# Kernel tuning notes

Hardware: AMD Instinct MI355X
Metric: run time of the kernel (lower is better)

Reference implementation:

```python
import jax, jax.numpy as jnp
import numpy as np

NUM_GROUPS = 8
NUM_HEADS = 8
EPS = 1e-5


def setup_inputs() -> dict:
    key = jax.random.key(0)
    k1, k2, k3 = jax.random.split(key, 3)
    b, c, h, w = 16, 512, 32, 32
    x = jax.random.normal(k1, (b, c, h, w), dtype=jnp.float32)
    gn_w = jnp.ones((c,), dtype=jnp.float32)
    gn_b = jnp.zeros((c,), dtype=jnp.float32)
    qkv_w = jax.random.normal(k2, (3 * c, c), dtype=jnp.float32) * (1.0 / np.sqrt(c))
    qkv_b = jnp.zeros((3 * c,), dtype=jnp.float32)
    proj_w = jax.random.normal(k3, (c, c), dtype=jnp.float32) * (1.0 / np.sqrt(c))
    proj_b = jnp.zeros((c,), dtype=jnp.float32)
    return {"x": x, "gn_w": gn_w, "gn_b": gn_b, "qkv_w": qkv_w,
            "qkv_b": qkv_b, "proj_w": proj_w, "proj_b": proj_b}


def reference(x, gn_w, gn_b, qkv_w, qkv_b, proj_w, proj_b):
    b, c, h, w = x.shape
    H = NUM_HEADS
    d = c // H
    N = h * w
    scale = d ** (-0.5)

    # GroupNorm(8, c), affine
    xg = x.reshape(b, NUM_GROUPS, -1)
    mu = xg.mean(axis=-1, keepdims=True)
    var = xg.var(axis=-1, keepdims=True)
    xn = ((xg - mu) * jax.lax.rsqrt(var + EPS)).reshape(b, c, h, w)
    xn = xn * gn_w[None, :, None, None] + gn_b[None, :, None, None]

    # 1x1 conv qkv: [b, 3c, h, w]
    qkv = jnp.einsum('oc,bchw->bohw', qkv_w, xn) + qkv_b[None, :, None, None]
    # 'b (three h d) x y -> three b h (x y) d'
    qkv = qkv.reshape(b, 3, H, d, N)          # (b, 3, H, d, N)
    q = jnp.swapaxes(qkv[:, 0], -1, -2)       # (b, H, N, d)
    k = jnp.swapaxes(qkv[:, 1], -1, -2)
    v = jnp.swapaxes(qkv[:, 2], -1, -2)

    attn = jnp.einsum('bhid,bhjd->bhij', q, k) * scale
    attn = jax.nn.softmax(attn, axis=-1)
    out = jnp.einsum('bhij,bhjd->bhid', attn, v)  # (b, H, N, d)

    # 'b h (x y) d -> b (h d) x y'
    out = jnp.swapaxes(out, -1, -2).reshape(b, c, h, w)
    out = jnp.einsum('oc,bchw->bohw', proj_w, out) + proj_b[None, :, None, None]
    return x + out
```

## Files before the change

kernel.cpp:

```cpp
#include <hip/hip_runtime.h>
#include <math.h>

typedef unsigned short u16;
typedef __attribute__((ext_vector_type(8))) short short8;
typedef __attribute__((ext_vector_type(4))) float floatx4;
typedef __attribute__((ext_vector_type(4))) u16 v4u16;
typedef __attribute__((ext_vector_type(8))) u16 v8u16;

#define B_   16
#define C_   512
#define NSP  1024
#define EPSV 1e-5f
#define QSCALE 0.18033688011117f

__device__ __forceinline__ u16 f2bf(float f) {
  union { float f; unsigned u; } v; v.f = f;
  unsigned r = v.u + 0x7FFFu + ((v.u >> 16) & 1u);
  return (u16)(r >> 16);
}

__device__ __forceinline__ void gld16(const u16* g, u16* l) {
  __builtin_amdgcn_global_load_lds(
      (const __attribute__((address_space(1))) void*)g,
      (__attribute__((address_space(3))) void*)l, 16, 0, 0);
}

__device__ __forceinline__ unsigned pk_bf(float a, float b) {
  return __builtin_amdgcn_perm(__float_as_uint(b), __float_as_uint(a), 0x07060302u);
}

__global__ __launch_bounds__(256) void cvt_bf16(
    const float* __restrict__ qa, u16* __restrict__ oa,
    const float* __restrict__ pa, u16* __restrict__ ob)
{
  int blk = blockIdx.x;
  const float* in; u16* out; int i;
  if (blk < 768) { in = qa; out = oa; i = (blk * 256 + threadIdx.x) * 4; }
  else           { in = pa; out = ob; i = ((blk - 768) * 256 + threadIdx.x) * 4; }
  float4 v = *(const float4*)(in + i);
  v4u16 o = { f2bf(v.x), f2bf(v.y), f2bf(v.z), f2bf(v.w) };
  *(v4u16*)(out + i) = o;
}

__global__ __launch_bounds__(256) void gn_stats(
    const float* __restrict__ x, float* __restrict__ stats)
{
  int blk = blockIdx.x;
  int bg = blk >> 3, ck = blk & 7;
  const float4* xp = (const float4*)(x + (((size_t)bg * 64 + ck * 8) * NSP));
  float s = 0.f, ss = 0.f;
#pragma unroll
  for (int it = 0; it < 8; ++it) {
    float4 v = xp[it * 256 + threadIdx.x];
    s  += v.x + v.y + v.z + v.w;
    ss += v.x * v.x + v.y * v.y + v.z * v.z + v.w * v.w;
  }
  for (int off = 32; off > 0; off >>= 1) {
    s  += __shfl_down(s, off);
    ss += __shfl_down(ss, off);
  }
  __shared__ float rs[4], rss[4];
  int lane = threadIdx.x & 63, wv = threadIdx.x >> 6;
  if (lane == 0) { rs[wv] = s; rss[wv] = ss; }
  __syncthreads();
  if (threadIdx.x == 0) {
    float S  = rs[0] + rs[1] + rs[2] + rs[3];
    float SS = rss[0] + rss[1] + rss[2] + rss[3];
    atomicAdd(&stats[bg * 2], S);
    atomicAdd(&stats[bg * 2 + 1], SS);
  }
}

__global__ __launch_bounds__(256) void gn_apply(
    const float* __restrict__ x, const float* __restrict__ stats,
    const float* __restrict__ gw, const float* __restrict__ gb,
    u16* __restrict__ xn)
{
  int blk = blockIdx.x;
  int bg = blk >> 4, nt = blk & 15;
  int b = bg >> 3, g = bg & 7;
  float S = stats[bg * 2], SS = stats[bg * 2 + 1];
  float mu  = S * (1.f / 65536.f);
  float var = SS * (1.f / 65536.f) - mu * mu;
  float inv = rsqrtf(var + EPSV);
  __shared__ float T[64][65];
  const float* xb = x + (size_t)bg * 64 * NSP;
  int t = threadIdx.x;
#pragma unroll
  for (int it = 0; it < 4; ++it) {
    int task = it * 256 + t;
    int cc = task >> 4, ns = task & 15;
    float4 v = *(const float4*)(xb + (size_t)cc * NSP + nt * 64 + ns * 4);
    T[cc][ns * 4 + 0] = v.x; T[cc][ns * 4 + 1] = v.y;
    T[cc][ns * 4 + 2] = v.z; T[cc][ns * 4 + 3] = v.w;
  }
  __syncthreads();
#pragma unroll
  for (int it = 0; it < 2; ++it) {
    int task = it * 256 + t;
    int n = task >> 3, cs = task & 7;
    v8u16 o;
#pragma unroll
    for (int u = 0; u < 8; ++u) {
      int cg = g * 64 + cs * 8 + u;
      float val = (T[cs * 8 + u][n] - mu) * inv * gw[cg] + gb[cg];
      o[u] = f2bf(val);
    }
    *(v8u16*)(xn + ((size_t)b * NSP + nt * 64 + n) * C_ + g * 64 + cs * 8) = o;
  }
}

template <int MODE>
__global__ __launch_bounds__(256) void gemm_mfma(
    const u16* __restrict__ W, const u16* __restrict__ X,
    const float* __restrict__ bias, const float* __restrict__ resid,
    u16* __restrict__ out_qk, u16* __restrict__ out_v,
    float* __restrict__ out_f)
{
  __shared__ u16 smem[17408];
  u16* As = smem;
  u16* Bs = smem + 4096;
  int id = blockIdx.x;
  int yb = id >> 7, rr = id & 127;
  int b = rr >> 3, xb_ = rr & 7;
  int m0 = yb * 128, n0 = xb_ * 128;
  int t = threadIdx.x, lane = t & 63, w = t >> 6;
  int c = lane & 15, q = lane >> 4;
  int wm = w >> 1, wn = w & 1;
  const u16* Xb = X + (size_t)b * NSP * C_;

  floatx4 acc[4][4];
#pragma unroll
  for (int mi = 0; mi < 4; ++mi)
#pragma unroll
    for (int ni = 0; ni < 4; ++ni) acc[mi][ni] = (floatx4){0.f, 0.f, 0.f, 0.f};

  for (int k0 = 0; k0 < 512; k0 += 32) {
    __syncthreads();
#pragma unroll
    for (int it = 0; it < 2; ++it) {
      int task = it * 256 + t;
      int mr = task >> 2;
      int gk = (task & 3) ^ ((mr >> 1) & 3);
      gld16(W + (size_t)(m0 + mr) * C_ + k0 + gk * 8, As + task * 8);
    }
#pragma unroll
    for (int it = 0; it < 2; ++it) {
      int task = it * 256 + t;
      int nr = task >> 2;
      int gk = (task & 3) ^ ((nr >> 1) & 3);
      gld16(Xb + (size_t)(n0 + nr) * C_ + k0 + gk * 8, Bs + task * 8);
    }
    __syncthreads();
    short8 af[4], bfr[4];
#pragma unroll
    for (int mi = 0; mi < 4; ++mi) {
      int m = wm * 64 + mi * 16 + c;
      af[mi] = *(const short8*)(As + m * 32 + ((q ^ ((m >> 1) & 3)) << 3));
    }
#pragma unroll
    for (int ni = 0; ni < 4; ++ni) {
      int n = wn * 64 + ni * 16 + c;
      bfr[ni] = *(const short8*)(Bs + n * 32 + ((q ^ ((n >> 1) & 3)) << 3));
    }
#pragma unroll
    for (int mi = 0; mi < 4; ++mi)
#pragma unroll
      for (int ni = 0; ni < 4; ++ni)
        acc[mi][ni] = __builtin_amdgcn_mfma_f32_16x16x32_bf16(
            af[mi], bfr[ni], acc[mi][ni], 0, 0, 0);
  }
  __syncthreads();

  if (MODE == 0) {
    if (m0 < 1024) {
      float sc = (m0 < 512) ? QSCALE : 1.0f;
      u16* Cl = smem;
#pragma unroll
      for (int mi = 0; mi < 4; ++mi) {
        floatx4 bi = *(const floatx4*)(bias + m0 + wm * 64 + mi * 16 + q * 4);
#pragma unroll
        for (int ni = 0; ni < 4; ++ni) {
          int n = wn * 64 + ni * 16 + c;
          int m = wm * 64 + mi * 16 + q * 4;
          v4u16 pk;
#pragma unroll
          for (int r = 0; r < 4; ++r) pk[r] = f2bf((acc[mi][ni][r] + bi[r]) * sc);
          *(v4u16*)(Cl + n * 136 + m) = pk;
        }
      }
      __syncthreads();
#pragma unroll
      for (int it = 0; it < 8; ++it) {
        int task = it * 256 + t;
        int n = task >> 4, seg = task & 15;
        v8u16 v = *(const v8u16*)(Cl + n * 136 + seg * 8);
        *(v8u16*)(out_qk + ((size_t)b * NSP + n0 + n) * 1024 + m0 + seg * 8) = v;
      }
    } else {
      u16* Cl = smem;
#pragma unroll
      for (int mi = 0; mi < 4; ++mi) {
        floatx4 bi = *(const floatx4*)(bias + m0 + wm * 64 + mi * 16 + q * 4);
#pragma unroll
        for (int ni = 0; ni < 4; ++ni) {
          int n = wn * 64 + ni * 16 + c;
          int m = wm * 64 + mi * 16 + q * 4;
#pragma unroll
          for (int r = 0; r < 4; ++r)
            Cl[(m + r) * 136 + n] = f2bf(acc[mi][ni][r] + bi[r]);
        }
      }
      __syncthreads();
#pragma unroll
      for (int it = 0; it < 8; ++it) {
        int task = it * 256 + t;
        int m = task >> 4, seg = task & 15;
        v8u16 v = *(const v8u16*)(Cl + m * 136 + seg * 8);
        *(v8u16*)(out_v + ((size_t)b * C_ + m0 - 1024 + m) * NSP + n0 + seg * 8) = v;
      }
    }
  } else {
#pragma unroll
    for (int mi = 0; mi < 4; ++mi) {
      floatx4 bi = *(const floatx4*)(bias + m0 + wm * 64 + mi * 16 + q * 4);
#pragma unroll
      for (int ni = 0; ni < 4; ++ni) {
        int n = n0 + wn * 64 + ni * 16 + c;
        int m = m0 + wm * 64 + mi * 16 + q * 4;
#pragma unroll
        for (int r = 0; r < 4; ++r) {
          size_t o = ((size_t)b * C_ + m + r) * NSP + n;
          out_f[o] = acc[mi][ni][r] + bi[r] + resid[o];
        }
      }
    }
  }
}

__global__ __launch_bounds__(256, 4) void attn_mfma(
    const u16* __restrict__ qk, const u16* __restrict__ vbuf,
    u16* __restrict__ att)
{
  __shared__ u16 __align__(16) smem[16384];
  int id = blockIdx.x;
  int hb = id & 127;
  int i0 = id >> 7;
  int h = hb >> 4, b = hb & 15;
  int t = threadIdx.x, lane = t & 63, w = t >> 6;
  int c = lane & 15, q = lane >> 4;
  const u16* qbase = qk + (size_t)b * NSP * 1024;
  const u16* vbase = vbuf + (size_t)(b * C_ + h * 64) * NSP;

#pragma unroll
  for (int it = 0; it < 4; ++it) {
    int task = it * 256 + t;
    int r = task >> 3, seg = task & 7, ds = (seg ^ (r & 7)) * 8;
    gld16(qbase + (size_t)(i0 * 128 + r) * 1024 + h * 64 + ds, smem + task * 8);
  }
#pragma unroll
  for (int it = 0; it < 2; ++it) {
    int task = it * 256 + t;
    int r = task >> 3, seg = task & 7, ds = (seg ^ (r & 7)) * 8;
    gld16(qbase + (size_t)r * 1024 + 512 + h * 64 + ds, smem + 8192 + task * 8);
    gld16(vbase + (size_t)r * NSP + ds, smem + 12288 + task * 8);
  }
  __syncthreads();

  short8 qa[2][2];
#pragma unroll
  for (int nf = 0; nf < 2; ++nf) {
    int row = w * 32 + nf * 16 + c;
#pragma unroll
    for (int ch = 0; ch < 2; ++ch)
      qa[nf][ch] = *(const short8*)(smem + row * 64 + (((q + 4 * ch) ^ (c & 7)) << 3));
  }
  __syncthreads();

  floatx4 Oacc[4][2];
#pragma unroll
  for (int dt = 0; dt < 4; ++dt)
#pragma unroll
    for (int nf = 0; nf < 2; ++nf) Oacc[dt][nf] = (floatx4){0.f, 0.f, 0.f, 0.f};
  float tsum[2] = {0.f, 0.f};

  for (int j0 = 0; j0 < 16; ++j0) {
    int p = j0 & 1;
    u16* KS = smem + (p ? 0 : 8192);
    u16* VS = KS + 4096;
    if (j0 < 15) {
      u16* KN = smem + (p ? 8192 : 0);
      u16* VN = KN + 4096;
#pragma unroll
      for (int it = 0; it < 2; ++it) {
        int task = it * 256 + t;
        int r = task >> 3, seg = task & 7, ds = (seg ^ (r & 7)) * 8;
        gld16(qbase + (size_t)((j0 + 1) * 64 + r) * 1024 + 512 + h * 64 + ds,
              KN + task * 8);
        gld16(vbase + (size_t)r * NSP + (j0 + 1) * 64 + ds, VN + task * 8);
      }
    }
    unsigned pk2[4][2][2];
#pragma unroll
    for (int jt = 0; jt < 4; ++jt) {
      int row = jt * 16 + c;
      short8 kb0 = *(const short8*)(KS + row * 64 + ((q ^ (row & 7)) << 3));
      short8 kb1 = *(const short8*)(KS + row * 64 + (((q + 4) ^ (row & 7)) << 3));
#pragma unroll
      for (int nf = 0; nf < 2; ++nf) {
        floatx4 z = (floatx4){0.f, 0.f, 0.f, 0.f};
        z = __builtin_amdgcn_mfma_f32_16x16x32_bf16(kb0, qa[nf][0], z, 0, 0, 0);
        z = __builtin_amdgcn_mfma_f32_16x16x32_bf16(kb1, qa[nf][1], z, 0, 0, 0);
        float p0 = __builtin_amdgcn_exp2f(z[0]);
        float p1 = __builtin_amdgcn_exp2f(z[1]);
        float p2 = __builtin_amdgcn_exp2f(z[2]);
        float p3 = __builtin_amdgcn_exp2f(z[3]);
        tsum[nf] += (p0 + p1) + (p2 + p3);
        pk2[jt][nf][0] = pk_bf(p0, p1);
        pk2[jt][nf][1] = pk_bf(p2, p3);
      }
    }
#pragma unroll
    for (int jt2 = 0; jt2 < 2; ++jt2) {
      short8 pf[2];
#pragma unroll
      for (int nf = 0; nf < 2; ++nf) {
        union { short8 s; unsigned d[4]; } u;
        u.d[0] = pk2[2 * jt2][nf][0];     u.d[1] = pk2[2 * jt2][nf][1];
        u.d[2] = pk2[2 * jt2 + 1][nf][0]; u.d[3] = pk2[2 * jt2 + 1][nf][1];
        pf[nf] = u.s;
      }
      int s1 = jt2 * 4 + (q >> 1);
      int io = (q & 1) * 4;
#pragma unroll
      for (int dt = 0; dt < 4; ++dt) {
        int dd = dt * 16 + c;
        union { short8 s; unsigned long long d[2]; } vf;
        vf.d[0] = *(const unsigned long long*)(
            VS + dd * 64 + ((s1 ^ (c & 7)) << 3) + io);
        vf.d[1] = *(const unsigned long long*)(
            VS + dd * 64 + (((s1 + 2) ^ (c & 7)) << 3) + io);
#pragma unroll
        for (int nf = 0; nf < 2; ++nf)
          Oacc[dt][nf] = __builtin_amdgcn_mfma_f32_16x16x32_bf16(
              vf.s, pf[nf], Oacc[dt][nf], 0, 0, 0);
      }
    }
    __syncthreads();
  }

#pragma unroll
  for (int nf = 0; nf < 2; ++nf) {
    tsum[nf] += __shfl_xor(tsum[nf], 16);
    tsum[nf] += __shfl_xor(tsum[nf], 32);
    float rinv = 1.f / tsum[nf];
    int n = i0 * 128 + w * 32 + nf * 16 + c;
#pragma unroll
    for (int dt = 0; dt < 4; ++dt) {
      v4u16 pk;
#pragma unroll
      for (int r = 0; r < 4; ++r) pk[r] = f2bf(Oacc[dt][nf][r] * rinv);
      *(v4u16*)(att + ((size_t)b * NSP + n) * C_ + h * 64 + dt * 16 + q * 4) = pk;
    }
  }
}

extern "C" void kernel_launch(void* const* d_in, const int* in_sizes, int n_in,
                              void* d_out, int out_size, void* d_ws, size_t ws_size,
                              hipStream_t stream)
{
  const float* x    = (const float*)d_in[0];
  const float* gw   = (const float*)d_in[1];
  const float* gb   = (const float*)d_in[2];
  const float* qkvw = (const float*)d_in[3];
  const float* qkvb = (const float*)d_in[4];
  const float* pw   = (const float*)d_in[5];
  const float* pb   = (const float*)d_in[6];
  float* out = (float*)d_out;

  u16* xn    = (u16*)d_ws;
  u16* qkb   = xn   + 8388608;
  u16* vbf   = qkb  + 16777216;
  u16* attb  = vbf  + 8388608;
  u16* wq    = attb + 8388608;
  u16* wp    = wq   + 786432;
  float* stats = (float*)(wp + 262144);

  hipMemsetAsync(stats, 0, 128 * 2 * sizeof(float), stream);
  cvt_bf16<<<1024, 256, 0, stream>>>(qkvw, wq, pw, wp);
  gn_stats<<<1024, 256, 0, stream>>>(x, stats);
  gn_apply<<<2048, 256, 0, stream>>>(x, stats, gw, gb, xn);
  gemm_mfma<0><<<dim3(1536), 256, 0, stream>>>(
      wq, xn, qkvb, nullptr, qkb, vbf, nullptr);
  attn_mfma<<<dim3(1024), 256, 0, stream>>>(qkb, vbf, attb);
  gemm_mfma<1><<<dim3(512), 256, 0, stream>>>(
      wp, attb, pb, x, nullptr, nullptr, out);
}
```

Measured before the change: 208.9 us.

## Permute V layout at store time, compute softmax sums via MFMA with ones

The QKV GEMM epilogue now writes V columns in a permuted order within each 64-wide block, so the attention kernel can load each V fragment with a single 16-byte LDS read instead of two 8-byte reads. The softmax row sum is computed by an extra MFMA of the bf16 probabilities against a ones vector, replacing per-lane scalar adds and the cross-lane shuffles. The QK/exp phase is interleaved per half-tile with the PV MFMAs, and s_setprio raises wave priority around the MFMA block. The denominator now sums bf16-rounded probabilities, which matches the numerator but changes numerics slightly, and the global stores of V become two 8-byte writes.

After: 199.9 us. 1.05x faster.

```diff
diff --git a/kernel.cpp b/kernel.cpp
--- a/kernel.cpp
+++ b/kernel.cpp
@@ -216,8 +216,14 @@
       for (int it = 0; it < 8; ++it) {
         int task = it * 256 + t;
         int m = task >> 4, seg = task & 15;
+        int g64 = seg >> 3, s = seg & 7;
+        int k0 = ((s & 4) << 3) | ((s & 1) << 4) | ((s & 2) << 1);
         v8u16 v = *(const v8u16*)(Cl + m * 136 + seg * 8);
-        *(v8u16*)(out_v + ((size_t)b * C_ + m0 - 1024 + m) * NSP + n0 + seg * 8) = v;
+        v4u16 lo = { v[0], v[1], v[2], v[3] };
+        v4u16 hi = { v[4], v[5], v[6], v[7] };
+        size_t base = ((size_t)b * C_ + m0 - 1024 + m) * NSP + n0 + g64 * 64;
+        *(v4u16*)(out_v + base + k0) = lo;
+        *(v4u16*)(out_v + base + k0 + 8) = hi;
       }
     }
   } else {
@@ -277,12 +283,18 @@
   }
   __syncthreads();
 
+  short8 onesf;
+#pragma unroll
+  for (int u = 0; u < 8; ++u) onesf[u] = (short)0x3F80;
+
   floatx4 Oacc[4][2];
+  floatx4 OaccT[2];
 #pragma unroll
   for (int dt = 0; dt < 4; ++dt)
 #pragma unroll
     for (int nf = 0; nf < 2; ++nf) Oacc[dt][nf] = (floatx4){0.f, 0.f, 0.f, 0.f};
-  float tsum[2] = {0.f, 0.f};
+#pragma unroll
+  for (int nf = 0; nf < 2; ++nf) OaccT[nf] = (floatx4){0.f, 0.f, 0.f, 0.f};
 
   for (int j0 = 0; j0 < 16; ++j0) {
     int p = j0 & 1;
@@ -300,60 +312,59 @@
         gld16(vbase + (size_t)r * NSP + (j0 + 1) * 64 + ds, VN + task * 8);
       }
     }
-    unsigned pk2[4][2][2];
-#pragma unroll
-    for (int jt = 0; jt < 4; ++jt) {
-      int row = jt * 16 + c;
-      short8 kb0 = *(const short8*)(KS + row * 64 + ((q ^ (row & 7)) << 3));
-      short8 kb1 = *(const short8*)(KS + row * 64 + (((q + 4) ^ (row & 7)) << 3));
-#pragma unroll
-      for (int nf = 0; nf < 2; ++nf) {
-        floatx4 z = (floatx4){0.f, 0.f, 0.f, 0.f};
-        z = __builtin_amdgcn_mfma_f32_16x16x32_bf16(kb0, qa[nf][0], z, 0, 0, 0);
-        z = __builtin_amdgcn_mfma_f32_16x16x32_bf16(kb1, qa[nf][1], z, 0, 0, 0);
-        float p0 = __builtin_amdgcn_exp2f(z[0]);
-        float p1 = __builtin_amdgcn_exp2f(z[1]);
-        float p2 = __builtin_amdgcn_exp2f(z[2]);
-        float p3 = __builtin_amdgcn_exp2f(z[3]);
-        tsum[nf] += (p0 + p1) + (p2 + p3);
-        pk2[jt][nf][0] = pk_bf(p0, p1);
-        pk2[jt][nf][1] = pk_bf(p2, p3);
-      }
-    }
 #pragma unroll
     for (int jt2 = 0; jt2 < 2; ++jt2) {
+      unsigned pk2[2][2][2];
+#pragma unroll
+      for (int jj = 0; jj < 2; ++jj) {
+        int jt = jt2 * 2 + jj;
+        int row = jt * 16 + c;
+        short8 kb0 = *(const short8*)(KS + row * 64 + ((q ^ (row & 7)) << 3));
+        short8 kb1 = *(const short8*)(KS + row * 64 + (((q + 4) ^ (row & 7)) << 3));
+#pragma unroll
+        for (int nf = 0; nf < 2; ++nf) {
+          floatx4 z = (floatx4){0.f, 0.f, 0.f, 0.f};
+          z = __builtin_amdgcn_mfma_f32_16x16x32_bf16(kb0, qa[nf][0], z, 0, 0, 0);
+          z = __builtin_amdgcn_mfma_f32_16x16x32_bf16(kb1, qa[nf][1], z, 0, 0, 0);
+          float p0 = __builtin_amdgcn_exp2f(z[0]);
+          float p1 = __builtin_amdgcn_exp2f(z[1]);
+          float p2 = __builtin_amdgcn_exp2f(z[2]);
+          float p3 = __builtin_amdgcn_exp2f(z[3]);
+          pk2[jj][nf][0] = pk_bf(p0, p1);
+          pk2[jj][nf][1] = pk_bf(p2, p3);
+        }
+      }
       short8 pf[2];
 #pragma unroll
       for (int nf = 0; nf < 2; ++nf) {
         union { short8 s; unsigned d[4]; } u;
-        u.d[0] = pk2[2 * jt2][nf][0];     u.d[1] = pk2[2 * jt2][nf][1];
-        u.d[2] = pk2[2 * jt2 + 1][nf][0]; u.d[3] = pk2[2 * jt2 + 1][nf][1];
+        u.d[0] = pk2[0][nf][0]; u.d[1] = pk2[0][nf][1];
+        u.d[2] = pk2[1][nf][0]; u.d[3] = pk2[1][nf][1];
         pf[nf] = u.s;
       }
-      int s1 = jt2 * 4 + (q >> 1);
-      int io = (q & 1) * 4;
+      __builtin_amdgcn_s_setprio(1);
 #pragma unroll
       for (int dt = 0; dt < 4; ++dt) {
         int dd = dt * 16 + c;
-        union { short8 s; unsigned long long d[2]; } vf;
-        vf.d[0] = *(const unsigned long long*)(
-            VS + dd * 64 + ((s1 ^ (c & 7)) << 3) + io);
-        vf.d[1] = *(const unsigned long long*)(
-            VS + dd * 64 + (((s1 + 2) ^ (c & 7)) << 3) + io);
+        short8 vfr = *(const short8*)(
+            VS + dd * 64 + (((jt2 * 4 + q) ^ (dd & 7)) << 3));
 #pragma unroll
         for (int nf = 0; nf < 2; ++nf)
           Oacc[dt][nf] = __builtin_amdgcn_mfma_f32_16x16x32_bf16(
-              vf.s, pf[nf], Oacc[dt][nf], 0, 0, 0);
-      }
+              vfr, pf[nf], Oacc[dt][nf], 0, 0, 0);
+      }
+#pragma unroll
+      for (int nf = 0; nf < 2; ++nf)
+        OaccT[nf] = __builtin_amdgcn_mfma_f32_16x16x32_bf16(
+            onesf, pf[nf], OaccT[nf], 0, 0, 0);
+      __builtin_amdgcn_s_setprio(0);
     }
     __syncthreads();
   }
 
 #pragma unroll
   for (int nf = 0; nf < 2; ++nf) {
-    tsum[nf] += __shfl_xor(tsum[nf], 16);
-    tsum[nf] += __shfl_xor(tsum[nf], 32);
-    float rinv = 1.f / tsum[nf];
+    float rinv = 1.f / OaccT[nf][0];
     int n = i0 * 128 + w * 32 + nf * 16 + c;
 #pragma unroll
     for (int dt = 0; dt < 4; ++dt) {
```
